# Optimization experiments

Hardware: AMD Instinct MI355X
Metric: run time of the kernel (lower is better)

The kernel has to match this reference:

```python
import jax, jax.numpy as jnp
import numpy as np

# LeNet-5 custom connectivity between S2 (6 ch) and C3 (16 ch): MAP[i, o] = 1 if input ch i feeds output ch o
MAP_INFO = np.array([
    [1, 0, 0, 0, 1, 1, 1, 0, 0, 1, 1, 1, 1, 0, 1, 1],
    [1, 1, 0, 0, 0, 1, 1, 1, 0, 0, 1, 1, 1, 1, 0, 1],
    [1, 1, 1, 0, 0, 0, 1, 1, 1, 0, 0, 1, 0, 1, 1, 1],
    [0, 1, 1, 1, 0, 0, 1, 1, 1, 1, 0, 0, 1, 0, 1, 1],
    [0, 0, 1, 1, 1, 0, 0, 1, 1, 1, 1, 0, 1, 1, 0, 1],
    [0, 0, 0, 1, 1, 1, 0, 0, 1, 1, 1, 1, 0, 1, 1, 1],
], dtype=np.float32)  # [6, 16]

SCALE = 1.7159
SLOPE = 2.0 / 3.0


def _conv(x, w):
    # x: [B, Cin, H, W], w: [Cout, Cin, kh, kw], VALID padding, stride 1
    return jax.lax.conv_general_dilated(
        x, w, window_strides=(1, 1), padding='VALID',
        dimension_numbers=('NCHW', 'OIHW', 'NCHW'))


def _subsample(x, w, b):
    # 2x2 average pool then per-channel affine (trainable scale/bias)
    B, C, H, W = x.shape
    p = x.reshape(B, C, H // 2, 2, W // 2, 2).mean(axis=(3, 5))
    return p * w[None, :, None, None] + b[None, :, None, None]


def _act(x):
    return SCALE * jnp.tanh(SLOPE * x)


def setup_inputs() -> dict:
    key = jax.random.key(0)
    ks = jax.random.split(key, 16)
    B = 8192

    def unif(k, shape, fan_in):
        return (jax.random.uniform(k, shape, dtype=jnp.float32) * 4.8 - 2.4) / fan_in

    x = jax.random.normal(ks[0], (B, 1, 32, 32), dtype=jnp.float32)
    c1_w = unif(ks[1], (6, 1, 5, 5), 25 * 1)
    c1_b = jax.random.uniform(ks[2], (6,), dtype=jnp.float32) * 0.1
    s2_w = unif(ks[3], (6,), 4)
    s2_b = jax.random.uniform(ks[4], (6,), dtype=jnp.float32)
    c3_w = unif(ks[5], (16, 6, 5, 5), 25 * 6)
    c3_b = jax.random.uniform(ks[6], (16,), dtype=jnp.float32) * 0.1
    s4_w = unif(ks[7], (16,), 4)
    s4_b = jax.random.uniform(ks[8], (16,), dtype=jnp.float32)
    c5_w = unif(ks[9], (120, 16, 5, 5), 25 * 16)
    c5_b = jax.random.uniform(ks[10], (120,), dtype=jnp.float32) * 0.1
    f6_w = unif(ks[11], (84, 120), 120)
    f6_b = jax.random.uniform(ks[12], (84,), dtype=jnp.float32) * 0.1
    rbf_w = jax.random.uniform(ks[13], (84, 10), dtype=jnp.float32)
    return dict(x=x, c1_w=c1_w, c1_b=c1_b, s2_w=s2_w, s2_b=s2_b,
                c3_w=c3_w, c3_b=c3_b, s4_w=s4_w, s4_b=s4_b,
                c5_w=c5_w, c5_b=c5_b, f6_w=f6_w, f6_b=f6_b, rbf_w=rbf_w)


def reference(x, c1_w, c1_b, s2_w, s2_b, c3_w, c3_b, s4_w, s4_b,
              c5_w, c5_b, f6_w, f6_b, rbf_w):
    # C1: 1->6 conv5, replicate padding 2 -> [B,6,32,32]
    xp = jnp.pad(x, ((0, 0), (0, 0), (2, 2), (2, 2)), mode='edge')
    h = _conv(xp, c1_w) + c1_b[None, :, None, None]
    # S2 + squashing act -> [B,6,16,16]
    h = _act(_subsample(h, s2_w, s2_b))
    # C3: sparse-connectivity conv expressed as dense conv with masked weights -> [B,16,12,12]
    mask = jnp.asarray(MAP_INFO.T)[:, :, None, None]  # [16,6,1,1]
    h = _conv(h, c3_w * mask) + c3_b[None, :, None, None]
    # S4 + act -> [B,16,6,6]
    h = _act(_subsample(h, s4_w, s4_b))
    # C5: 16->120 conv5 -> [B,120,1,1]
    h = _conv(h, c5_w) + c5_b[None, :, None, None]
    h = h.reshape(-1, 120)
    # F6 + act -> [B,84]
    h = _act(h @ f6_w.T + f6_b)
    # RBF output: squared euclidean distance to class prototypes -> [B,10]
    out = jnp.sum((h[:, :, None] - rbf_w[None, :, :]) ** 2, axis=1)
    return out
```

## Files before the change

### kernel.cpp

```cpp
#include <hip/hip_runtime.h>
#include <math.h>

typedef _Float16 h16;
typedef h16  h8v __attribute__((ext_vector_type(8)));
typedef h16  h4v __attribute__((ext_vector_type(4)));
typedef h16  h2v __attribute__((ext_vector_type(2)));
typedef float f4v __attribute__((ext_vector_type(4)));
typedef unsigned int u32;

#if defined(__has_builtin)
#if __has_builtin(__builtin_amdgcn_fdot2)
#define FDOT2(a,b,c) __builtin_amdgcn_fdot2((a),(b),(c),false)
#endif
#endif
#ifndef FDOT2
#define FDOT2(a,b,c) ((c) + (float)(a).x*(float)(b).x + (float)(a).y*(float)(b).y)
#endif

#define WS_K1H  0
#define WS_B1   216
#define WS_B3   224
#define WS_W3H  240
#define WS_W5H  2544
#define WS_F6H  29168
#define WS_RBFT 35312

#define L_B3    0
#define L_C5B   64
#define L_F6B   544
#define L_S2H   880
#define L_A5    880
#define L_HB    880
#define L_XPAD  14704
#define L_S4    14704
#define L_A6    14704
#define LDS_TOTAL 20080

__device__ const unsigned char MASK16[16] = {7,14,28,56,49,35,15,30,60,57,51,39,27,54,45,63};

__device__ __forceinline__ float squash(float x) {
    float E = __expf(1.33333333f * x);
    return 1.7159f - 3.4318f * __builtin_amdgcn_rcpf(1.0f + E);
}

__global__ __launch_bounds__(256) void prep_kernel(
    const float* __restrict__ c1_w, const float* __restrict__ c1_b,
    const float* __restrict__ s2_w, const float* __restrict__ s2_b,
    const float* __restrict__ c3_w, const float* __restrict__ c3_b,
    const float* __restrict__ s4_w, const float* __restrict__ s4_b,
    const float* __restrict__ c5_w, const float* __restrict__ f6_w,
    const float* __restrict__ rbf_w,
    float* __restrict__ ws)
{
    const int gid = blockIdx.x * 256 + threadIdx.x;
    const int gstr = gridDim.x * 256;
    h16* K1H = (h16*)ws;
    for (int idx = gid; idx < 216; idx += gstr) {
        int c = idx / 36, r = idx - c * 36;
        int u = r / 6, v = r - u * 6;
        float s = 0.f;
        #pragma unroll
        for (int dy = 0; dy < 2; ++dy)
            #pragma unroll
            for (int dx = 0; dx < 2; ++dx) {
                int ky = u - dy, kx = v - dx;
                if (ky >= 0 && ky < 5 && kx >= 0 && kx < 5)
                    s += c1_w[(c * 5 + ky) * 5 + kx];
            }
        K1H[idx] = (h16)(0.25f * s * s2_w[c]);
    }
    if (gid < 6)  ws[WS_B1 + gid] = s2_w[gid] * c1_b[gid] + s2_b[gid];
    if (gid < 16) ws[WS_B3 + gid] = s4_w[gid] * c3_b[gid] + s4_b[gid];
    h16* W3H = (h16*)(ws + WS_W3H);
    for (int idx = gid; idx < 4608; idx += gstr) {
        int i = idx / 768, r = idx - i * 768;
        int n = r / 48, k = r - n * 48;
        float val = 0.f;
        if (k < 36) {
            int u = k / 6, v = k - u * 6;
            float s = 0.f;
            #pragma unroll
            for (int dy = 0; dy < 2; ++dy)
                #pragma unroll
                for (int dx = 0; dx < 2; ++dx) {
                    int ky = u - dy, kx = v - dx;
                    if (ky >= 0 && ky < 5 && kx >= 0 && kx < 5)
                        s += c3_w[((n * 6 + i) * 5 + ky) * 5 + kx];
                }
            val = ((MASK16[n] >> i) & 1) ? 0.25f * s4_w[n] * s : 0.f;
        }
        W3H[idx] = (h16)val;
    }
    h16* W5H = (h16*)(ws + WS_W5H);
    for (int idx = gid; idx < 53248; idx += gstr) {
        int kb = idx >> 12, r = idx & 4095;
        int n = r >> 5, k = r & 31;
        int kg = kb * 32 + k;
        float val = (n < 120 && kg < 400) ? c5_w[n * 400 + kg] : 0.f;
        W5H[idx] = (h16)val;
    }
    h16* F6H = (h16*)(ws + WS_F6H);
    for (int idx = gid; idx < 12288; idx += gstr) {
        int n = idx >> 7, k = idx & 127;
        float val = (n < 84 && k < 120) ? f6_w[n * 120 + k] : 0.f;
        F6H[idx] = (h16)val;
    }
    for (int idx = gid; idx < 840; idx += gstr) {
        int k = idx / 10, c = idx - k * 10;
        ws[WS_RBFT + c * 84 + k] = rbf_w[idx];
    }
}

__global__ __launch_bounds__(256, 8) void lenet_kernel(
    const float* __restrict__ x,
    const float* __restrict__ c5_b, const float* __restrict__ f6_b,
    const float* __restrict__ ws,
    float* __restrict__ out)
{
    __shared__ __align__(16) char smem[LDS_TOTAL];
    float* s_b3  = (float*)(smem + L_B3);
    float* s_c5b = (float*)(smem + L_C5B);
    float* s_f6b = (float*)(smem + L_F6B);
    h16*  XPAD   = (h16*)(smem + L_XPAD);
    h16*  S2H    = (h16*)(smem + L_S2H);
    h16*  S4     = (h16*)(smem + L_S4);
    h16*  A5     = (h16*)(smem + L_A5);
    h16*  A6     = (h16*)(smem + L_A6);
    float* HB    = (float*)(smem + L_HB);

    const int tid  = threadIdx.x;
    const int wave = __builtin_amdgcn_readfirstlane(tid >> 6);
    const int lane = tid & 63;
    const int quad = lane >> 4;
    const int lr   = lane & 15;

    if (tid < 16)  s_b3[tid] = ws[WS_B3 + tid];
    if (tid < 120) s_c5b[tid] = c5_b[tid];
    if (tid < 84)  s_f6b[tid] = f6_b[tid];
    const float* xb = x + (size_t)blockIdx.x * 4096;
    h2v r1[6];
    #pragma unroll
    for (int it = 0; it < 6; ++it) {
        int idx = tid + it * 256;
        if (idx < 1296) {
            int img2 = idx / 648, r2 = idx - img2 * 648;
            int u = r2 / 18, v = r2 - u * 18;
            int sy = min(max(u - 2, 0), 31);
            int c0 = min(max(2 * v - 2, 0), 31);
            int c1 = min(max(2 * v - 1, 0), 31);
            const float* xr0 = xb + img2 * 1024 + sy * 32;
            h2v hv0; hv0.x = (h16)xr0[c0]; hv0.y = (h16)xr0[c1];
            *(h2v*)(XPAD + img2 * 1296 + u * 36 + 2 * v) = hv0;
            const float* xr1 = xr0 + 2048;
            h2v hv1; hv1.x = (h16)xr1[c0]; hv1.y = (h16)xr1[c1];
            r1[it] = hv1;
        }
    }
    __syncthreads();

    {
        int py = tid & 15, px = tid >> 4;
        const h2v* K1H = (const h2v*)ws;
        #pragma unroll 1
        for (int img2 = 0; img2 < 2; ++img2) {
            const h16* basep = XPAD + img2 * 1296 + (2 * py) * 36 + 2 * px;
            h2v win2[18];
            #pragma unroll
            for (int u = 0; u < 6; ++u)
                #pragma unroll
                for (int p = 0; p < 3; ++p)
                    win2[u * 3 + p] = *(const h2v*)(basep + u * 36 + 2 * p);
            #pragma unroll
            for (int c = 0; c < 6; ++c) {
                float acc = ws[WS_B1 + c];
                #pragma unroll
                for (int j = 0; j < 18; ++j)
                    acc = FDOT2(win2[j], K1H[c * 18 + j], acc);
                S2H[img2 * 1728 + c * 288 + py * 18 + px] = (h16)squash(acc);
            }
        }
    }
    __syncthreads();

    #pragma unroll
    for (int it = 0; it < 6; ++it) {
        int idx = tid + it * 256;
        if (idx < 1296) {
            int img2 = idx / 648, r2 = idx - img2 * 648;
            int u = r2 / 18, v = r2 - u * 18;
            *(h2v*)(XPAD + img2 * 1296 + u * 36 + 2 * v) = r1[it];
        }
    }
    __syncthreads();

    {
        int py = tid & 15, px = tid >> 4;
        const h2v* K1H = (const h2v*)ws;
        #pragma unroll 1
        for (int img2 = 0; img2 < 2; ++img2) {
            const h16* basep = XPAD + img2 * 1296 + (2 * py) * 36 + 2 * px;
            h2v win2[18];
            #pragma unroll
            for (int u = 0; u < 6; ++u)
                #pragma unroll
                for (int p = 0; p < 3; ++p)
                    win2[u * 3 + p] = *(const h2v*)(basep + u * 36 + 2 * p);
            #pragma unroll
            for (int c = 0; c < 6; ++c) {
                float acc = ws[WS_B1 + c];
                #pragma unroll
                for (int j = 0; j < 18; ++j)
                    acc = FDOT2(win2[j], K1H[c * 18 + j], acc);
                S2H[(2 + img2) * 1728 + c * 288 + py * 18 + px] = (h16)squash(acc);
            }
        }
    }
    __syncthreads();

    {
        const h16* W3H = (const h16*)(ws + WS_W3H);
        int o0, o1, o2, o3;
        {
            int k0 = 8 * quad;
            int u0 = k0 / 6, v0 = k0 - u0 * 6;  o0 = u0 * 18 + v0;
            int k1 = k0 + 2;
            int u1 = k1 / 6, v1 = k1 - u1 * 6;  o1 = u1 * 18 + v1;
            int k2 = k0 + 4;
            int u2 = k2 / 6, v2 = k2 - u2 * 6;  o2 = u2 * 18 + v2;
            int k3 = k0 + 6;
            int u3 = k3 / 6, v3 = k3 - u3 * 6;  o3 = u3 * 18 + v3;
        }
        int baseh0, baseh1, baseh2;
        {
            int m0 = wave * 16 + lr;
            int i0 = m0 / 36, p0 = m0 - i0 * 36;
            baseh0 = i0 * 1728 + (2 * (p0 / 6)) * 18 + 2 * (p0 % 6);
            int m1 = (wave + 4) * 16 + lr;
            int i1 = m1 / 36, p1 = m1 - i1 * 36;
            baseh1 = i1 * 1728 + (2 * (p1 / 6)) * 18 + 2 * (p1 % 6);
            int m2 = 128 + lr;
            int i2 = m2 / 36, p2 = m2 - i2 * 36;
            baseh2 = i2 * 1728 + (2 * (p2 / 6)) * 18 + 2 * (p2 % 6);
        }
        f4v cacc0 = {}, cacc1 = {}, cacc2 = {};
        const bool w0 = (wave == 0);
        #pragma unroll
        for (int i = 0; i < 6; ++i) {
            const h16* bbase = W3H + i * 768 + lr * 48;
            h8v w3a = *(const h8v*)(bbase + quad * 8);
            h4v w3b = *(const h4v*)(bbase + 32 + quad * 4);
            const h16* bp0 = S2H + baseh0 + i * 288;
            {
                union { u32 u[4]; h8v h; } av;
                av.u[0] = *(const u32*)(bp0 + o0);
                av.u[1] = *(const u32*)(bp0 + o1);
                av.u[2] = *(const u32*)(bp0 + o2);
                av.u[3] = *(const u32*)(bp0 + o3);
                cacc0 = __builtin_amdgcn_mfma_f32_16x16x32_f16(av.h, w3a, cacc0, 0, 0, 0);
                union { u32 u[2]; h4v h; } av2;
                av2.u[0] = *(const u32*)(bp0 + 92);
                av2.u[1] = *(const u32*)(bp0 + 94);
                cacc0 = __builtin_amdgcn_mfma_f32_16x16x16f16(av2.h, w3b, cacc0, 0, 0, 0);
            }
            const h16* bp1 = S2H + baseh1 + i * 288;
            {
                union { u32 u[4]; h8v h; } av;
                av.u[0] = *(const u32*)(bp1 + o0);
                av.u[1] = *(const u32*)(bp1 + o1);
                av.u[2] = *(const u32*)(bp1 + o2);
                av.u[3] = *(const u32*)(bp1 + o3);
                cacc1 = __builtin_amdgcn_mfma_f32_16x16x32_f16(av.h, w3a, cacc1, 0, 0, 0);
                union { u32 u[2]; h4v h; } av2;
                av2.u[0] = *(const u32*)(bp1 + 92);
                av2.u[1] = *(const u32*)(bp1 + 94);
                cacc1 = __builtin_amdgcn_mfma_f32_16x16x16f16(av2.h, w3b, cacc1, 0, 0, 0);
            }
            if (w0) {
                const h16* bp2 = S2H + baseh2 + i * 288;
                union { u32 u[4]; h8v h; } av;
                av.u[0] = *(const u32*)(bp2 + o0);
                av.u[1] = *(const u32*)(bp2 + o1);
                av.u[2] = *(const u32*)(bp2 + o2);
                av.u[3] = *(const u32*)(bp2 + o3);
                cacc2 = __builtin_amdgcn_mfma_f32_16x16x32_f16(av.h, w3a, cacc2, 0, 0, 0);
                union { u32 u[2]; h4v h; } av2;
                av2.u[0] = *(const u32*)(bp2 + 92);
                av2.u[1] = *(const u32*)(bp2 + 94);
                cacc2 = __builtin_amdgcn_mfma_f32_16x16x16f16(av2.h, w3b, cacc2, 0, 0, 0);
            }
        }
        float b3v = s_b3[lr];
        {
            #pragma unroll
            for (int r = 0; r < 4; ++r) {
                int m = wave * 16 + quad * 4 + r;
                int img = m / 36, pos = m - img * 36;
                S4[img * 672 + lr * 42 + pos] = (h16)squash(cacc0[r] + b3v);
            }
            #pragma unroll
            for (int r = 0; r < 4; ++r) {
                int m = (wave + 4) * 16 + quad * 4 + r;
                int img = m / 36, pos = m - img * 36;
                S4[img * 672 + lr * 42 + pos] = (h16)squash(cacc1[r] + b3v);
            }
            if (w0) {
                #pragma unroll
                for (int r = 0; r < 4; ++r) {
                    int m = 128 + quad * 4 + r;
                    int img = m / 36, pos = m - img * 36;
                    S4[img * 672 + lr * 42 + pos] = (h16)squash(cacc2[r] + b3v);
                }
            }
        }
    }
    __syncthreads();

    {
        {
            int m = tid >> 4, i = tid & 15;
            int img = m >> 2, q = m & 3, qy = q >> 1, qx = q & 1;
            const h16* s4b = S4 + img * 672 + i * 42 + qy * 6 + qx;
            h16* dst = A5 + m * 424 + i * 25;
            #pragma unroll
            for (int k = 0; k < 25; ++k)
                dst[k] = s4b[(k / 5) * 6 + (k % 5)];
            if (i == 15) {
                #pragma unroll
                for (int j = 0; j < 12; ++j)
                    *(u32*)(A5 + m * 424 + 400 + 2 * j) = 0u;
            }
        }
        __syncthreads();
        const h16* W5H = (const h16*)(ws + WS_W5H);
        f4v dacc0 = {}, dacc1 = {};
        #pragma unroll
        for (int i = 0; i < 13; ++i) {
            h8v bf0 = *(const h8v*)(W5H + i * 4096 + (wave * 32 + lr) * 32 + quad * 8);
            h8v bf1 = *(const h8v*)(W5H + i * 4096 + (wave * 32 + 16 + lr) * 32 + quad * 8);
            h8v af0 = *(const h8v*)(A5 + lr * 424 + i * 32 + quad * 8);
            dacc0 = __builtin_amdgcn_mfma_f32_16x16x32_f16(af0, bf0, dacc0, 0, 0, 0);
            dacc1 = __builtin_amdgcn_mfma_f32_16x16x32_f16(af0, bf1, dacc1, 0, 0, 0);
        }
        if (tid < 64) {
            int m = tid >> 2, j = tid & 3;
            *(u32*)(A6 + m * 136 + 120 + 2 * j) = 0u;
        }
        {
            int n0 = wave * 32 + lr;
            if (n0 < 120) {
                int tt = n0 / 30, cb = (n0 - tt * 30) * 4;
                float bias = s_c5b[n0];
                #pragma unroll
                for (int r = 0; r < 4; ++r) {
                    int m = quad * 4 + r;
                    A6[((m >> 2) * 4 + tt) * 136 + cb + (m & 3)] = (h16)(dacc0[r] + bias);
                }
            }
            int n1 = wave * 32 + 16 + lr;
            if (n1 < 120) {
                int tt = n1 / 30, cb = (n1 - tt * 30) * 4;
                float bias = s_c5b[n1];
                #pragma unroll
                for (int r = 0; r < 4; ++r) {
                    int m = quad * 4 + r;
                    A6[((m >> 2) * 4 + tt) * 136 + cb + (m & 3)] = (h16)(dacc1[r] + bias);
                }
            }
        }
    }
    __syncthreads();

    {
        const h16* F6H = (const h16*)(ws + WS_F6H);
        f4v eacc0 = {}, eacc1 = {};
        const bool w2 = (wave < 2);
        #pragma unroll
        for (int kc = 0; kc < 4; ++kc) {
            h8v a8 = *(const h8v*)(A6 + lr * 136 + kc * 32 + quad * 8);
            h8v b0 = *(const h8v*)(F6H + (wave * 16 + lr) * 128 + kc * 32 + quad * 8);
            eacc0 = __builtin_amdgcn_mfma_f32_16x16x32_f16(a8, b0, eacc0, 0, 0, 0);
            if (w2) {
                h8v b1 = *(const h8v*)(F6H + ((wave + 4) * 16 + lr) * 128 + kc * 32 + quad * 8);
                eacc1 = __builtin_amdgcn_mfma_f32_16x16x32_f16(a8, b1, eacc1, 0, 0, 0);
            }
        }
        {
            int n = wave * 16 + lr;
            float bias = s_f6b[n];
            #pragma unroll
            for (int r = 0; r < 4; ++r) {
                int m = quad * 4 + r;
                HB[m * 88 + n] = squash(eacc0[r] + bias);
            }
        }
        if (w2) {
            int n = (wave + 4) * 16 + lr;
            if (n < 84) {
                float bias = s_f6b[n];
                #pragma unroll
                for (int r = 0; r < 4; ++r) {
                    int m = quad * 4 + r;
                    HB[m * 88 + n] = squash(eacc1[r] + bias);
                }
            }
        }
    }
    __syncthreads();

    if (tid < 160) {
        int m = tid / 10, cls = tid - m * 10;
        const float4* hr = (const float4*)(HB + m * 88);
        const float4* pr = (const float4*)(ws + WS_RBFT + cls * 84);
        float a = 0.f;
        #pragma unroll
        for (int u = 0; u < 21; ++u) {
            float4 hv = hr[u], pv = pr[u];
            float dx = hv.x - pv.x, dy = hv.y - pv.y;
            float dz = hv.z - pv.z, dw = hv.w - pv.w;
            a += dx * dx + dy * dy + dz * dz + dw * dw;
        }
        out[(size_t)blockIdx.x * 160 + tid] = a;
    }
}

extern "C" void kernel_launch(void* const* d_in, const int* in_sizes, int n_in,
                              void* d_out, int out_size, void* d_ws, size_t ws_size,
                              hipStream_t stream) {
    (void)n_in; (void)out_size; (void)ws_size;
    const float* x     = (const float*)d_in[0];
    const float* c1_w  = (const float*)d_in[1];
    const float* c1_b  = (const float*)d_in[2];
    const float* s2_w  = (const float*)d_in[3];
    const float* s2_b  = (const float*)d_in[4];
    const float* c3_w  = (const float*)d_in[5];
    const float* c3_b  = (const float*)d_in[6];
    const float* s4_w  = (const float*)d_in[7];
    const float* s4_b  = (const float*)d_in[8];
    const float* c5_w  = (const float*)d_in[9];
    const float* c5_b  = (const float*)d_in[10];
    const float* f6_w  = (const float*)d_in[11];
    const float* f6_b  = (const float*)d_in[12];
    const float* rbf_w = (const float*)d_in[13];
    float* out = (float*)d_out;
    float* ws  = (float*)d_ws;

    const int B = in_sizes[0] / 1024;

    prep_kernel<<<256, 256, 0, stream>>>(c1_w, c1_b, s2_w, s2_b, c3_w, c3_b,
                                         s4_w, s4_b, c5_w, f6_w, rbf_w, ws);
    lenet_kernel<<<B / 4, 256, 0, stream>>>(x, c5_b, f6_b, ws, out);
}
```

Before: 138.2 us.

## Move C1/S2 conv onto MFMA and load input with vectorized float4 staging

Replaces the per-thread fdot2 C1+S2 convolution with MFMA 16x16x32 and 16x16x16 tiles, using a folded 6x6 kernel padded to 48 K and 16 output channels. Input images are now staged with coalesced float4 loads plus a separate edge-replication pass, instead of clamped scalar gathers held in registers. C5 weights and A5 activations are repacked to a 26-stride per channel so the A5 build writes packed 32-bit words rather than single halves. Biases are folded into the MFMA accumulator initial values. The MFMA path wastes 10 of 16 output columns and a quarter of K, and adds an extra sync-separated stage pass.

Result: faster. 135.1 us (-2.2%).

```diff
diff --git a/kernel.cpp b/kernel.cpp
--- a/kernel.cpp
+++ b/kernel.cpp
@@ -8,22 +8,13 @@
 typedef float f4v __attribute__((ext_vector_type(4)));
 typedef unsigned int u32;
 
-#if defined(__has_builtin)
-#if __has_builtin(__builtin_amdgcn_fdot2)
-#define FDOT2(a,b,c) __builtin_amdgcn_fdot2((a),(b),(c),false)
-#endif
-#endif
-#ifndef FDOT2
-#define FDOT2(a,b,c) ((c) + (float)(a).x*(float)(b).x + (float)(a).y*(float)(b).y)
-#endif
-
-#define WS_K1H  0
-#define WS_B1   216
-#define WS_B3   224
-#define WS_W3H  240
-#define WS_W5H  2544
-#define WS_F6H  29168
-#define WS_RBFT 35312
+#define WS_B1   0
+#define WS_B3   8
+#define WS_KB1  24
+#define WS_W3H  408
+#define WS_W5H  2712
+#define WS_F6H  29336
+#define WS_RBFT 35480
 
 #define L_B3    0
 #define L_C5B   64
@@ -54,23 +45,27 @@
 {
     const int gid = blockIdx.x * 256 + threadIdx.x;
     const int gstr = gridDim.x * 256;
-    h16* K1H = (h16*)ws;
-    for (int idx = gid; idx < 216; idx += gstr) {
-        int c = idx / 36, r = idx - c * 36;
-        int u = r / 6, v = r - u * 6;
-        float s = 0.f;
-        #pragma unroll
-        for (int dy = 0; dy < 2; ++dy)
-            #pragma unroll
-            for (int dx = 0; dx < 2; ++dx) {
-                int ky = u - dy, kx = v - dx;
-                if (ky >= 0 && ky < 5 && kx >= 0 && kx < 5)
-                    s += c1_w[(c * 5 + ky) * 5 + kx];
-            }
-        K1H[idx] = (h16)(0.25f * s * s2_w[c]);
-    }
     if (gid < 6)  ws[WS_B1 + gid] = s2_w[gid] * c1_b[gid] + s2_b[gid];
     if (gid < 16) ws[WS_B3 + gid] = s4_w[gid] * c3_b[gid] + s4_b[gid];
+    h16* KB1 = (h16*)(ws + WS_KB1);
+    for (int idx = gid; idx < 768; idx += gstr) {
+        int n = idx / 48, k = idx - n * 48;
+        float val = 0.f;
+        if (n < 6 && k < 36) {
+            int u = k / 6, v = k - u * 6;
+            float s = 0.f;
+            #pragma unroll
+            for (int dy = 0; dy < 2; ++dy)
+                #pragma unroll
+                for (int dx = 0; dx < 2; ++dx) {
+                    int ky = u - dy, kx = v - dx;
+                    if (ky >= 0 && ky < 5 && kx >= 0 && kx < 5)
+                        s += c1_w[(n * 5 + ky) * 5 + kx];
+                }
+            val = 0.25f * s * s2_w[n];
+        }
+        KB1[idx] = (h16)val;
+    }
     h16* W3H = (h16*)(ws + WS_W3H);
     for (int idx = gid; idx < 4608; idx += gstr) {
         int i = idx / 768, r = idx - i * 768;
@@ -93,10 +88,11 @@
     }
     h16* W5H = (h16*)(ws + WS_W5H);
     for (int idx = gid; idx < 53248; idx += gstr) {
-        int kb = idx >> 12, r = idx & 4095;
-        int n = r >> 5, k = r & 31;
+        int kb = idx >> 12, rr = idx & 4095;
+        int n = rr >> 5, k = rr & 31;
         int kg = kb * 32 + k;
-        float val = (n < 120 && kg < 400) ? c5_w[n * 400 + kg] : 0.f;
+        int i = kg / 26, r = kg - i * 26;
+        float val = (n < 120 && r < 25) ? c5_w[n * 400 + i * 25 + r] : 0.f;
         W5H[idx] = (h16)val;
     }
     h16* F6H = (h16*)(ws + WS_F6H);
@@ -138,83 +134,80 @@
     if (tid < 120) s_c5b[tid] = c5_b[tid];
     if (tid < 84)  s_f6b[tid] = f6_b[tid];
     const float* xb = x + (size_t)blockIdx.x * 4096;
-    h2v r1[6];
-    #pragma unroll
-    for (int it = 0; it < 6; ++it) {
-        int idx = tid + it * 256;
-        if (idx < 1296) {
-            int img2 = idx / 648, r2 = idx - img2 * 648;
-            int u = r2 / 18, v = r2 - u * 18;
-            int sy = min(max(u - 2, 0), 31);
-            int c0 = min(max(2 * v - 2, 0), 31);
-            int c1 = min(max(2 * v - 1, 0), 31);
-            const float* xr0 = xb + img2 * 1024 + sy * 32;
-            h2v hv0; hv0.x = (h16)xr0[c0]; hv0.y = (h16)xr0[c1];
-            *(h2v*)(XPAD + img2 * 1296 + u * 36 + 2 * v) = hv0;
-            const float* xr1 = xr0 + 2048;
-            h2v hv1; hv1.x = (h16)xr1[c0]; hv1.y = (h16)xr1[c1];
-            r1[it] = hv1;
-        }
-    }
-    __syncthreads();
-
+    const h16* KB1 = (const h16*)(ws + WS_KB1);
+    h8v w1a = *(const h8v*)(KB1 + lr * 48 + quad * 8);
+    h4v w1b = *(const h4v*)(KB1 + lr * 48 + 32 + quad * 4);
+    float b1v = ws[WS_B1 + (lr < 6 ? lr : 0)];
+    int oB0, oB1, oB2, oB3;
     {
-        int py = tid & 15, px = tid >> 4;
-        const h2v* K1H = (const h2v*)ws;
-        #pragma unroll 1
-        for (int img2 = 0; img2 < 2; ++img2) {
-            const h16* basep = XPAD + img2 * 1296 + (2 * py) * 36 + 2 * px;
-            h2v win2[18];
-            #pragma unroll
-            for (int u = 0; u < 6; ++u)
-                #pragma unroll
-                for (int p = 0; p < 3; ++p)
-                    win2[u * 3 + p] = *(const h2v*)(basep + u * 36 + 2 * p);
-            #pragma unroll
-            for (int c = 0; c < 6; ++c) {
-                float acc = ws[WS_B1 + c];
-                #pragma unroll
-                for (int j = 0; j < 18; ++j)
-                    acc = FDOT2(win2[j], K1H[c * 18 + j], acc);
-                S2H[img2 * 1728 + c * 288 + py * 18 + px] = (h16)squash(acc);
-            }
-        }
-    }
-    __syncthreads();
-
-    #pragma unroll
-    for (int it = 0; it < 6; ++it) {
-        int idx = tid + it * 256;
-        if (idx < 1296) {
-            int img2 = idx / 648, r2 = idx - img2 * 648;
-            int u = r2 / 18, v = r2 - u * 18;
-            *(h2v*)(XPAD + img2 * 1296 + u * 36 + 2 * v) = r1[it];
-        }
-    }
-    __syncthreads();
-
-    {
-        int py = tid & 15, px = tid >> 4;
-        const h2v* K1H = (const h2v*)ws;
-        #pragma unroll 1
-        for (int img2 = 0; img2 < 2; ++img2) {
-            const h16* basep = XPAD + img2 * 1296 + (2 * py) * 36 + 2 * px;
-            h2v win2[18];
-            #pragma unroll
-            for (int u = 0; u < 6; ++u)
-                #pragma unroll
-                for (int p = 0; p < 3; ++p)
-                    win2[u * 3 + p] = *(const h2v*)(basep + u * 36 + 2 * p);
-            #pragma unroll
-            for (int c = 0; c < 6; ++c) {
-                float acc = ws[WS_B1 + c];
-                #pragma unroll
-                for (int j = 0; j < 18; ++j)
-                    acc = FDOT2(win2[j], K1H[c * 18 + j], acc);
-                S2H[(2 + img2) * 1728 + c * 288 + py * 18 + px] = (h16)squash(acc);
-            }
-        }
-    }
+        int k0 = 8 * quad;      oB0 = (k0 / 6) * 36 + (k0 % 6);
+        int k1 = 8 * quad + 2;  oB1 = (k1 / 6) * 36 + (k1 % 6);
+        int k2 = 8 * quad + 4;  oB2 = (k2 / 6) * 36 + (k2 % 6);
+        int k3 = 8 * quad + 6;  oB3 = (k3 / 6) * 36 + (k3 % 6);
+    }
+
+    auto stageA = [&](int s) {
+        #pragma unroll
+        for (int k = 0; k < 2; ++k) {
+            int idx = tid + k * 256;
+            int im = idx >> 8;
+            int r  = (idx >> 3) & 31;
+            int c4 = idx & 7;
+            float4 v = *(const float4*)(xb + (2 * s + im) * 1024 + r * 32 + c4 * 4);
+            h2v p0; p0.x = (h16)v.x; p0.y = (h16)v.y;
+            h2v p1; p1.x = (h16)v.z; p1.y = (h16)v.w;
+            h16* d = XPAD + im * 1296 + (r + 2) * 36 + (4 * c4 + 2);
+            *(h2v*)(d)     = p0;
+            *(h2v*)(d + 2) = p1;
+        }
+        #pragma unroll
+        for (int k = 0; k < 3; ++k) {
+            int e = tid + k * 256;
+            if (e < 544) {
+                int im = (e >= 272) ? 1 : 0;
+                int h = e - 272 * im;
+                int u, v;
+                if (h < 144) { int q = h / 36; u = (q < 2) ? q : 32 + q; v = h - q * 36; }
+                else { int g = h - 144; u = 2 + (g >> 2); int q = g & 3; v = (q < 2) ? q : 32 + q; }
+                int sr = min(max(u - 2, 0), 31), sc = min(max(v - 2, 0), 31);
+                XPAD[im * 1296 + u * 36 + v] = (h16)xb[(2 * s + im) * 1024 + sr * 32 + sc];
+            }
+        }
+    };
+
+    auto stageB = [&](int s) {
+        const h16* bp = XPAD + (wave >> 1) * 1296 + (wave & 1) * 576 + 2 * lr;
+        h16* s2base = S2H + (s * 2 + (wave >> 1)) * 1728 + lr * 288 + (wave & 1) * 144 + quad * 4;
+        #pragma unroll
+        for (int tt = 0; tt < 8; ++tt) {
+            union { u32 u[4]; h8v h; } av;
+            av.u[0] = *(const u32*)(bp + oB0);
+            av.u[1] = *(const u32*)(bp + oB1);
+            av.u[2] = *(const u32*)(bp + oB2);
+            av.u[3] = *(const u32*)(bp + oB3);
+            f4v acc = {b1v, b1v, b1v, b1v};
+            acc = __builtin_amdgcn_mfma_f32_16x16x32_f16(av.h, w1a, acc, 0, 0, 0);
+            union { u32 u[2]; h4v h; } av2;
+            av2.u[0] = *(const u32*)(bp + 182);
+            av2.u[1] = *(const u32*)(bp + 184);
+            acc = __builtin_amdgcn_mfma_f32_16x16x16f16(av2.h, w1b, acc, 0, 0, 0);
+            if (lr < 6) {
+                h2v q0; q0.x = (h16)squash(acc[0]); q0.y = (h16)squash(acc[1]);
+                h2v q1; q1.x = (h16)squash(acc[2]); q1.y = (h16)squash(acc[3]);
+                *(h2v*)(s2base + tt * 18)     = q0;
+                *(h2v*)(s2base + tt * 18 + 2) = q1;
+            }
+            bp += 72;
+        }
+    };
+
+    stageA(0);
+    __syncthreads();
+    stageB(0);
+    __syncthreads();
+    stageA(1);
+    __syncthreads();
+    stageB(1);
     __syncthreads();
 
     {
@@ -242,7 +235,9 @@
             int i2 = m2 / 36, p2 = m2 - i2 * 36;
             baseh2 = i2 * 1728 + (2 * (p2 / 6)) * 18 + 2 * (p2 % 6);
         }
-        f4v cacc0 = {}, cacc1 = {}, cacc2 = {};
+        float b3v = s_b3[lr];
+        f4v cinit = {b3v, b3v, b3v, b3v};
+        f4v cacc0 = cinit, cacc1 = cinit, cacc2 = cinit;
         const bool w0 = (wave == 0);
         #pragma unroll
         for (int i = 0; i < 6; ++i) {
@@ -289,26 +284,25 @@
                 cacc2 = __builtin_amdgcn_mfma_f32_16x16x16f16(av2.h, w3b, cacc2, 0, 0, 0);
             }
         }
-        float b3v = s_b3[lr];
         {
             #pragma unroll
             for (int r = 0; r < 4; ++r) {
                 int m = wave * 16 + quad * 4 + r;
                 int img = m / 36, pos = m - img * 36;
-                S4[img * 672 + lr * 42 + pos] = (h16)squash(cacc0[r] + b3v);
+                S4[img * 672 + lr * 42 + pos] = (h16)squash(cacc0[r]);
             }
             #pragma unroll
             for (int r = 0; r < 4; ++r) {
                 int m = (wave + 4) * 16 + quad * 4 + r;
                 int img = m / 36, pos = m - img * 36;
-                S4[img * 672 + lr * 42 + pos] = (h16)squash(cacc1[r] + b3v);
+                S4[img * 672 + lr * 42 + pos] = (h16)squash(cacc1[r]);
             }
             if (w0) {
                 #pragma unroll
                 for (int r = 0; r < 4; ++r) {
                     int m = 128 + quad * 4 + r;
                     int img = m / 36, pos = m - img * 36;
-                    S4[img * 672 + lr * 42 + pos] = (h16)squash(cacc2[r] + b3v);
+                    S4[img * 672 + lr * 42 + pos] = (h16)squash(cacc2[r]);
                 }
             }
         }
@@ -320,19 +314,28 @@
             int m = tid >> 4, i = tid & 15;
             int img = m >> 2, q = m & 3, qy = q >> 1, qx = q & 1;
             const h16* s4b = S4 + img * 672 + i * 42 + qy * 6 + qx;
-            h16* dst = A5 + m * 424 + i * 25;
-            #pragma unroll
-            for (int k = 0; k < 25; ++k)
-                dst[k] = s4b[(k / 5) * 6 + (k % 5)];
-            if (i == 15) {
-                #pragma unroll
-                for (int j = 0; j < 12; ++j)
-                    *(u32*)(A5 + m * 424 + 400 + 2 * j) = 0u;
+            u32* dst = (u32*)(A5 + m * 424 + i * 26);
+            #pragma unroll
+            for (int w = 0; w < 12; ++w) {
+                int k0 = 2 * w, k1 = 2 * w + 1;
+                union { h2v h; u32 u; } p;
+                p.h.x = s4b[(k0 / 5) * 6 + (k0 % 5)];
+                p.h.y = s4b[(k1 / 5) * 6 + (k1 % 5)];
+                dst[w] = p.u;
+            }
+            {
+                union { h2v h; u32 u; } p;
+                p.h.x = s4b[28];
+                p.h.y = (h16)0.f;
+                dst[12] = p.u;
             }
         }
         __syncthreads();
         const h16* W5H = (const h16*)(ws + WS_W5H);
-        f4v dacc0 = {}, dacc1 = {};
+        float c5b0 = s_c5b[wave * 32 + lr];
+        float c5b1 = s_c5b[wave * 32 + 16 + lr];
+        f4v dacc0 = {c5b0, c5b0, c5b0, c5b0};
+        f4v dacc1 = {c5b1, c5b1, c5b1, c5b1};
         #pragma unroll
         for (int i = 0; i < 13; ++i) {
             h8v bf0 = *(const h8v*)(W5H + i * 4096 + (wave * 32 + lr) * 32 + quad * 8);
@@ -349,21 +352,19 @@
             int n0 = wave * 32 + lr;
             if (n0 < 120) {
                 int tt = n0 / 30, cb = (n0 - tt * 30) * 4;
-                float bias = s_c5b[n0];
                 #pragma unroll
                 for (int r = 0; r < 4; ++r) {
                     int m = quad * 4 + r;
-                    A6[((m >> 2) * 4 + tt) * 136 + cb + (m & 3)] = (h16)(dacc0[r] + bias);
+                    A6[((m >> 2) * 4 + tt) * 136 + cb + (m & 3)] = (h16)dacc0[r];
                 }
             }
             int n1 = wave * 32 + 16 + lr;
             if (n1 < 120) {
                 int tt = n1 / 30, cb = (n1 - tt * 30) * 4;
-                float bias = s_c5b[n1];
                 #pragma unroll
                 for (int r = 0; r < 4; ++r) {
                     int m = quad * 4 + r;
-                    A6[((m >> 2) * 4 + tt) * 136 + cb + (m & 3)] = (h16)(dacc1[r] + bias);
+                    A6[((m >> 2) * 4 + tt) * 136 + cb + (m & 3)] = (h16)dacc1[r];
                 }
             }
         }
@@ -372,8 +373,15 @@
 
     {
         const h16* F6H = (const h16*)(ws + WS_F6H);
-        f4v eacc0 = {}, eacc1 = {};
+        float f60 = s_f6b[wave * 16 + lr];
+        f4v eacc0 = {f60, f60, f60, f60};
+        f4v eacc1 = {};
         const bool w2 = (wave < 2);
+        if (w2) {
+            int n1 = (wave + 4) * 16 + lr;
+            float f61 = (n1 < 84) ? s_f6b[n1] : 0.f;
+            eacc1[0] = f61; eacc1[1] = f61; eacc1[2] = f61; eacc1[3] = f61;
+        }
         #pragma unroll
         for (int kc = 0; kc < 4; ++kc) {
             h8v a8 = *(const h8v*)(A6 + lr * 136 + kc * 32 + quad * 8);
@@ -386,21 +394,19 @@
         }
         {
             int n = wave * 16 + lr;
-            float bias = s_f6b[n];
             #pragma unroll
             for (int r = 0; r < 4; ++r) {
                 int m = quad * 4 + r;
-                HB[m * 88 + n] = squash(eacc0[r] + bias);
+                HB[m * 88 + n] = squash(eacc0[r]);
             }
         }
         if (w2) {
             int n = (wave + 4) * 16 + lr;
             if (n < 84) {
-                float bias = s_f6b[n];
                 #pragma unroll
                 for (int r = 0; r < 4; ++r) {
                     int m = quad * 4 + r;
-                    HB[m * 88 + n] = squash(eacc1[r] + bias);
+                    HB[m * 88 + n] = squash(eacc1[r]);
                 }
             }
         }
```
